# Optimization experiments

Measured on AMD Instinct MI355X. Metric: run time of the kernel, lower is better.

The kernel has to match this reference:

```python
import jax, jax.numpy as jnp
import numpy as np

AXIAL_WEIGHT = 1.0
N_NODES = 1_000_000
N_ELEM = 2_000_000


def setup_inputs() -> dict:
    key = jax.random.key(0)
    ks = jax.random.split(key, 12)
    N, E = N_NODES, N_ELEM
    pred_raw = jax.random.normal(ks[0], (N, 3), jnp.float32)
    u_c = jax.random.uniform(ks[1], (1,), jnp.float32) + 0.5
    theta_c = jax.random.uniform(ks[2], (1,), jnp.float32) + 0.5
    connectivity = jax.random.randint(ks[3], (E, 2), 0, N, jnp.int32)
    # lengths / section properties bounded away from zero (1/L^3 appears)
    elem_lengths = jax.random.uniform(ks[4], (E,), jnp.float32) + 0.5
    prop_E = jax.random.uniform(ks[5], (E,), jnp.float32) + 1.0
    prop_A = jax.random.uniform(ks[6], (E,), jnp.float32) + 0.5
    prop_I22 = jax.random.uniform(ks[7], (E,), jnp.float32) + 0.5
    ang = jax.random.uniform(ks[8], (E,), jnp.float32) * (2.0 * np.pi)
    # columns: [cos, 0, sin] -- forward reads cols 0 and 2
    elem_directions = jnp.stack([jnp.cos(ang), jnp.zeros_like(ang), jnp.sin(ang)], axis=1)
    F_ext = jax.random.normal(ks[9], (N, 3), jnp.float32)
    bc_disp = (jax.random.uniform(ks[10], (N, 1)) < 0.05).astype(jnp.float32)
    bc_rot = (jax.random.uniform(ks[11], (N, 1)) < 0.05).astype(jnp.float32)
    return {
        "pred_raw": pred_raw, "u_c": u_c, "theta_c": theta_c,
        "elem_lengths": elem_lengths, "prop_E": prop_E, "prop_A": prop_A,
        "prop_I22": prop_I22, "elem_directions": elem_directions,
        "F_ext": F_ext, "bc_disp": bc_disp, "bc_rot": bc_rot,
        "connectivity": connectivity,
    }


def reference(pred_raw, u_c, theta_c, elem_lengths, prop_E, prop_A, prop_I22,
              elem_directions, F_ext, bc_disp, bc_rot, connectivity):
    n_nodes = pred_raw.shape[0]
    # physical displacements: [ux*u_c, uz*u_c, th*theta_c]
    scale = jnp.concatenate([u_c, u_c, theta_c])  # [3]
    u_phys = pred_raw * scale[None, :]

    nA = connectivity[:, 0]
    nB = connectivity[:, 1]
    c = elem_directions[:, 0]
    s = elem_directions[:, 2]
    L = elem_lengths
    EA = prop_E * prop_A
    EI = prop_E * prop_I22

    uA = u_phys[nA]  # [E,3] gather
    uB = u_phys[nB]
    u_A = c * uA[:, 0] + s * uA[:, 1]
    w_A = -s * uA[:, 0] + c * uA[:, 1]
    th_A = -uA[:, 2]
    u_B = c * uB[:, 0] + s * uB[:, 1]
    w_B = -s * uB[:, 0] + c * uB[:, 1]
    th_B = -uB[:, 2]

    ea_l = EA / L * AXIAL_WEIGHT
    ei_l = EI / L
    ei_l2 = EI / L**2
    ei_l3 = EI / L**3

    # analytic K_loc @ d_local (K_loc is the standard 6x6 beam stiffness)
    dw = w_A - w_B
    f0 = ea_l * (u_A - u_B)
    f1 = 12.0 * ei_l3 * dw + 6.0 * ei_l2 * (th_A + th_B)
    f2 = 6.0 * ei_l2 * dw + 4.0 * ei_l * th_A + 2.0 * ei_l * th_B
    f3 = -f0
    f4 = -f1
    f5 = 6.0 * ei_l2 * dw + 2.0 * ei_l * th_A + 4.0 * ei_l * th_B

    fA = jnp.stack([c * f0 - s * f1, s * f0 + c * f1, -f2], axis=1)  # [E,3]
    fB = jnp.stack([c * f3 - s * f4, s * f3 + c * f4, -f5], axis=1)

    F_int = jax.ops.segment_sum(
        jnp.concatenate([fA, fB], axis=0),
        jnp.concatenate([nA, nB], axis=0),
        num_segments=n_nodes)  # [N,3] scatter-add

    R = F_int - F_ext
    free_mask = jnp.concatenate([1.0 - bc_disp, 1.0 - bc_disp, 1.0 - bc_rot], axis=1)
    R_free = R * free_mask
    F_free = F_ext * free_mask
    F_norm_sq = jnp.maximum(jnp.sum(F_free**2), 1e-30)
    loss = jnp.sum(R_free**2) / F_norm_sq  # single graph -> n_graphs = 1
    return loss
```

## Files before the change

kernel.cpp:

```cpp
#include <hip/hip_runtime.h>
#include <hip/hip_fp16.h>


#define SPANC  4096
#define NBC    256
#define CURP   4
#define FTH    1024
#define FBE    2048
#define CB     96
#define NCHUNK 4
#define BASEI  272
#define QSCALE 8192.0f
#define QINV   1.220703125e-4f

#define SMEM_BYTES 49408
#define FO_SLAB 0
#define FO_SBK  32768
#define FO_HIST 36864
#define FO_BOFF 37888
#define FO_AST  38912
#define FO_WSUM 39936
#define AO_TILE 0
#define AO_SN   49152
#define AO_SD   49280

__device__ __forceinline__ uint2 packrec(float fx, float fy, float fz, int local) {
    unsigned short hx = __half_as_ushort(__float2half(fx));
    unsigned short hy = __half_as_ushort(__float2half(fy));
    unsigned short hz = __half_as_ushort(__float2half(fz));
    return make_uint2(((unsigned)hy << 16) | hx, ((unsigned)local << 16) | hz);
}

__device__ __forceinline__ int block_incl_scan(int v, int* wsum, int lane, int wv) {
    #pragma unroll
    for (int off = 1; off < 64; off <<= 1) {
        int t = __shfl_up(v, off, 64);
        if (lane >= off) v += t;
    }
    if (lane == 63) wsum[wv] = v;
    __syncthreads();
    if (wv == 0) {
        int w = (lane < 16) ? wsum[lane] : 0;
        #pragma unroll
        for (int off = 1; off < 16; off <<= 1) {
            int t = __shfl_up(w, off, 64);
            if (lane >= off) w += t;
        }
        if (lane < 16) wsum[lane] = w;
    }
    __syncthreads();
    return v + ((wv > 0) ? wsum[wv - 1] : 0);
}

__global__ void __launch_bounds__(1024)
upcnt_kernel(const float* __restrict__ pred, const float* __restrict__ u_c,
             const float* __restrict__ theta_c, uint2* __restrict__ up,
             int N, int upG,
             const long long* __restrict__ conn, int* __restrict__ rows,
             int E, int CE) {
    __shared__ int h[NCHUNK][NBC];
    int tid = threadIdx.x;
    int bid = blockIdx.x;

    if (bid < upG) {
        int i = bid * 1024 + tid;
        if (i < N) {
            float uc = u_c[0], tc = theta_c[0];
            float x = __builtin_nontemporal_load(&pred[3 * i + 0]) * uc;
            float y = __builtin_nontemporal_load(&pred[3 * i + 1]) * uc;
            float z = __builtin_nontemporal_load(&pred[3 * i + 2]) * tc;
            unsigned hx = __half_as_ushort(__float2half(x));
            unsigned hy = __half_as_ushort(__float2half(y));
            unsigned hz = __half_as_ushort(__float2half(z));
            up[i] = make_uint2((hy << 16) | hx, hz);
        }
        return;
    }

    int blk = bid - upG;
    h[tid >> 8][tid & 255] = 0;
    __syncthreads();
    int stride = CB * 1024;
    int ce2 = 2 * CE, ce3 = 3 * CE;
    for (int e = blk * 1024 + tid; e < E; e += stride) {
        long long v = __builtin_nontemporal_load(conn + e);
        int na = (int)(unsigned)((unsigned long long)v & 0xFFFFFFFFull);
        int nb = (int)(unsigned)((unsigned long long)v >> 32);
        int c = (e >= ce2) ? ((e >= ce3) ? 3 : 2) : ((e >= CE) ? 1 : 0);
        atomicAdd(&h[c][na >> 12], 1);
        atomicAdd(&h[c][nb >> 12], 1);
    }
    __syncthreads();
    int c = tid >> 8, b = tid & 255;
    __builtin_nontemporal_store(h[c][b], &rows[(c * CB + blk) * NBC + b]);
}

__global__ void __launch_bounds__(1024)
scan4_kernel(const int* __restrict__ rows, int* __restrict__ cursors,
             int* __restrict__ bases, double* __restrict__ accSlots) {
    __shared__ int wsum[16];
    __shared__ int segend[NCHUNK];
    int tid = threadIdx.x, lane = tid & 63, wv = tid >> 6;
    int c = tid >> 8, b = tid & 255;
    int v = 0;
    #pragma unroll 4
    for (int r = 0; r < CB; ++r) v += rows[(c * CB + r) * NBC + b];
    int incl = block_incl_scan(v, wsum, lane, wv);
    if (b == 255) segend[c] = incl;
    __syncthreads();
    int segoff = (c > 0) ? segend[c - 1] : 0;
    int inclSeg = incl - segoff;
    int* base_c = bases + c * BASEI;
    base_c[b + 1] = inclSeg;
    if (b == 0) base_c[0] = 0;
    cursors[(c * NBC + b) * CURP] = inclSeg - v;
    if (tid < 512) accSlots[tid] = 0.0;
}

__device__ __forceinline__ void fill_body(
    char* smem,
    const long long* __restrict__ conn,
    const uint2* __restrict__ upk,
    const float* __restrict__ len,
    const float* __restrict__ pE,
    const float* __restrict__ pA,
    const float* __restrict__ pI,
    const float* __restrict__ dir,
    uint2* __restrict__ arena,
    int* __restrict__ cursor,
    int cs, int ce, int bid) {
    uint2*         slab   = (uint2*)(smem + FO_SLAB);
    unsigned char* sbk    = (unsigned char*)(smem + FO_SBK);
    int*           hist   = (int*)(smem + FO_HIST);
    int*           boff   = (int*)(smem + FO_BOFF);
    int*           astart = (int*)(smem + FO_AST);
    int*           wsum   = (int*)(smem + FO_WSUM);

    int tid = threadIdx.x, lane = tid & 63, wv = tid >> 6;
    if (tid < NBC) hist[tid] = 0;
    __syncthreads();

    int bs = cs + bid * FBE;
    int be = bs + FBE; if (be > ce) be = ce;

    unsigned sv[4];
    uint2    rc[4];

    #pragma unroll
    for (int j = 0; j < 2; ++j) {
        int e = bs + j * FTH + tid;
        unsigned sa = 0xFFFFFFFFu, sb = 0xFFFFFFFFu;
        if (e < be) {
            long long cv = __builtin_nontemporal_load(conn + e);
            int na = (int)(unsigned)((unsigned long long)cv & 0xFFFFFFFFull);
            int nb = (int)(unsigned)((unsigned long long)cv >> 32);

            uint2 ua = upk[na];
            uint2 ub = upk[nb];

            float c  = __builtin_nontemporal_load(&dir[3 * e + 0]);
            float s  = __builtin_nontemporal_load(&dir[3 * e + 2]);
            float L  = __builtin_nontemporal_load(&len[e]);
            float Ee = __builtin_nontemporal_load(&pE[e]);
            float EA = Ee * __builtin_nontemporal_load(&pA[e]);
            float EI = Ee * __builtin_nontemporal_load(&pI[e]);

            float a0 = __half2float(__ushort_as_half((unsigned short)(ua.x & 0xFFFFu)));
            float a1 = __half2float(__ushort_as_half((unsigned short)(ua.x >> 16)));
            float a2 = __half2float(__ushort_as_half((unsigned short)(ua.y & 0xFFFFu)));
            float b0 = __half2float(__ushort_as_half((unsigned short)(ub.x & 0xFFFFu)));
            float b1 = __half2float(__ushort_as_half((unsigned short)(ub.x >> 16)));
            float b2 = __half2float(__ushort_as_half((unsigned short)(ub.y & 0xFFFFu)));

            float u_A  =  c * a0 + s * a1;
            float w_A  = -s * a0 + c * a1;
            float th_A = -a2;
            float u_B  =  c * b0 + s * b1;
            float w_B  = -s * b0 + c * b1;
            float th_B = -b2;

            float invL  = 1.0f / L;
            float ea_l  = EA * invL;
            float ei_l  = EI * invL;
            float ei_l2 = ei_l  * invL;
            float ei_l3 = ei_l2 * invL;

            float dw = w_A - w_B;
            float f0 = ea_l * (u_A - u_B);
            float f1 = 12.0f * ei_l3 * dw + 6.0f * ei_l2 * (th_A + th_B);
            float f2 = 6.0f * ei_l2 * dw + 4.0f * ei_l * th_A + 2.0f * ei_l * th_B;
            float f5 = 6.0f * ei_l2 * dw + 2.0f * ei_l * th_A + 4.0f * ei_l * th_B;

            float fA0 = c * f0 - s * f1;
            float fA1 = s * f0 + c * f1;

            int bkA = na >> 12;
            int rA  = atomicAdd(&hist[bkA], 1);
            sa = ((unsigned)rA << 8) | (unsigned)bkA;
            rc[2 * j + 0] = packrec(fA0, fA1, -f2, na & 4095);

            int bkB = nb >> 12;
            int rB  = atomicAdd(&hist[bkB], 1);
            sb = ((unsigned)rB << 8) | (unsigned)bkB;
            rc[2 * j + 1] = packrec(-fA0, -fA1, -f5, nb & 4095);
        }
        sv[2 * j + 0] = sa;
        sv[2 * j + 1] = sb;
    }
    __syncthreads();

    int h = (tid < NBC) ? hist[tid] : 0;
    if (tid < NBC && h) astart[tid] = atomicAdd(&cursor[tid * CURP], h);
    int iT = block_incl_scan(h, wsum, lane, wv);
    if (tid < NBC) boff[tid] = iT - h;
    __syncthreads();

    #pragma unroll
    for (int r = 0; r < 4; ++r) {
        unsigned s2 = sv[r];
        if (s2 != 0xFFFFFFFFu) {
            int bk = (int)(s2 & 255u);
            int rk = (int)(s2 >> 8);
            int slot = boff[bk] + rk;
            slab[slot] = rc[r];
            sbk[slot]  = (unsigned char)bk;
        }
    }
    __syncthreads();

    int tot = boff[NBC - 1] + hist[NBC - 1];
    for (int i = tid; i < tot; i += FTH) {
        int bk = sbk[i];
        uint2 r2 = slab[i];
        unsigned long long v = ((unsigned long long)r2.y << 32) | (unsigned long long)r2.x;
        __builtin_nontemporal_store(v,
            (unsigned long long*)&arena[astart[bk] + (i - boff[bk])]);
    }
}

__device__ __forceinline__ void accum_body(
    char* smem,
    const unsigned long long* __restrict__ arena,
    const int* __restrict__ base,
    const float* __restrict__ Fext,
    const float* __restrict__ bcd,
    const float* __restrict__ bcr,
    double* __restrict__ accSlots,
    unsigned short* __restrict__ fint16,
    int N, int isFirst, int isLast, int b) {
    int*    tile = (int*)(smem + AO_TILE);
    double* sn   = (double*)(smem + AO_SN);
    double* sd   = (double*)(smem + AO_SD);

    int tid = threadIdx.x, lane = tid & 63, wv = tid >> 6;
    int nodeLo = b * SPANC;
    int gBase = nodeLo * 3;
    int gMax  = 3 * N;

    if (isFirst) {
        for (int i = tid; i < SPANC * 3; i += FTH) tile[i] = 0;
    } else {
        for (int i = tid; i < SPANC * 3; i += FTH) {
            int g = gBase + i;
            tile[i] = (g < gMax)
                ? __float2int_rn(__half2float(__ushort_as_half(
                      __builtin_nontemporal_load(&fint16[g]))) * QSCALE)
                : 0;
        }
    }
    __syncthreads();

    int s0 = base[b];
    int s1 = base[b + 1];
    for (int i = s0 + tid; i < s1; i += FTH) {
        unsigned long long rv = __builtin_nontemporal_load(arena + i);
        unsigned lo = (unsigned)(rv & 0xFFFFFFFFull);
        unsigned hi = (unsigned)(rv >> 32);
        float fx = __half2float(__ushort_as_half((unsigned short)(lo & 0xFFFFu)));
        float fy = __half2float(__ushort_as_half((unsigned short)(lo >> 16)));
        float fz = __half2float(__ushort_as_half((unsigned short)(hi & 0xFFFFu)));
        int local = (int)(hi >> 16);
        atomicAdd(&tile[local * 3 + 0], __float2int_rn(fx * QSCALE));
        atomicAdd(&tile[local * 3 + 1], __float2int_rn(fy * QSCALE));
        atomicAdd(&tile[local * 3 + 2], __float2int_rn(fz * QSCALE));
    }
    __syncthreads();

    if (!isLast) {
        for (int i = tid; i < SPANC * 3; i += FTH) {
            int g = gBase + i;
            if (g < gMax)
                __builtin_nontemporal_store(
                    __half_as_ushort(__float2half((float)tile[i] * QINV)),
                    &fint16[g]);
        }
        return;
    }

    int spanCnt = N - nodeLo;
    if (spanCnt > SPANC) spanCnt = SPANC;

    double num = 0.0, den = 0.0;
    for (int l = tid; l < spanCnt; l += FTH) {
        int n = nodeLo + l;
        float md = 1.0f - __builtin_nontemporal_load(&bcd[n]);
        float mr = 1.0f - __builtin_nontemporal_load(&bcr[n]);
        float e0 = __builtin_nontemporal_load(&Fext[3 * n + 0]);
        float e1 = __builtin_nontemporal_load(&Fext[3 * n + 1]);
        float e2 = __builtin_nontemporal_load(&Fext[3 * n + 2]);
        float t0 = (float)tile[l * 3 + 0] * QINV;
        float t1 = (float)tile[l * 3 + 1] * QINV;
        float t2 = (float)tile[l * 3 + 2] * QINV;
        float r0 = (t0 - e0) * md;
        float r1 = (t1 - e1) * md;
        float r2 = (t2 - e2) * mr;
        float g0 = e0 * md;
        float g1 = e1 * md;
        float g2 = e2 * mr;
        num += (double)r0 * r0 + (double)r1 * r1 + (double)r2 * r2;
        den += (double)g0 * g0 + (double)g1 * g1 + (double)g2 * g2;
    }
    #pragma unroll
    for (int off = 32; off > 0; off >>= 1) {
        num += __shfl_down(num, off, 64);
        den += __shfl_down(den, off, 64);
    }
    if (lane == 0) { sn[wv] = num; sd[wv] = den; }
    __syncthreads();
    if (tid == 0) {
        double tn = 0.0, td = 0.0;
        #pragma unroll
        for (int w = 0; w < 16; ++w) { tn += sn[w]; td += sd[w]; }
        double* slot = accSlots + (size_t)(b & 63) * 8;
        atomicAdd(&slot[0], tn);
        atomicAdd(&slot[1], td);
    }
}

__global__ void __launch_bounds__(1024)
fill_kernel(const long long* __restrict__ conn, const uint2* __restrict__ upk,
            const float* __restrict__ len, const float* __restrict__ pE,
            const float* __restrict__ pA, const float* __restrict__ pI,
            const float* __restrict__ dir, uint2* __restrict__ arena,
            int* __restrict__ cursor, int cs, int ce) {
    __shared__ __align__(16) char smem[SMEM_BYTES];
    fill_body(smem, conn, upk, len, pE, pA, pI, dir, arena, cursor, cs, ce,
              blockIdx.x);
}

__global__ void __launch_bounds__(1024)
accum_kernel(const unsigned long long* __restrict__ arena,
             const int* __restrict__ base, const float* __restrict__ Fext,
             const float* __restrict__ bcd, const float* __restrict__ bcr,
             double* __restrict__ accSlots, unsigned short* __restrict__ fint16,
             int N, int isFirst, int isLast) {
    __shared__ __align__(16) char smem[SMEM_BYTES];
    accum_body(smem, arena, base, Fext, bcd, bcr, accSlots, fint16, N,
               isFirst, isLast, blockIdx.x);
}

__global__ void __launch_bounds__(1024)
mid_kernel(const long long* __restrict__ conn, const uint2* __restrict__ upk,
           const float* __restrict__ len, const float* __restrict__ pE,
           const float* __restrict__ pA, const float* __restrict__ pI,
           const float* __restrict__ dir,
           uint2* __restrict__ arenaF, int* __restrict__ cursorF,
           int csF, int ceF, int NTF,
           const unsigned long long* __restrict__ arenaA,
           const int* __restrict__ baseA,
           const float* __restrict__ Fext, const float* __restrict__ bcd,
           const float* __restrict__ bcr, double* __restrict__ accSlots,
           unsigned short* __restrict__ fint16, int N, int isFirstA) {
    __shared__ __align__(16) char smem[SMEM_BYTES];
    if ((int)blockIdx.x < NTF)
        fill_body(smem, conn, upk, len, pE, pA, pI, dir, arenaF, cursorF,
                  csF, ceF, blockIdx.x);
    else
        accum_body(smem, arenaA, baseA, Fext, bcd, bcr, accSlots, fint16, N,
                   isFirstA, 0, blockIdx.x - NTF);
}

__global__ void final_kernel(const double* __restrict__ accSlots,
                             float* __restrict__ out) {
    int t = threadIdx.x;
    double n = accSlots[t * 8 + 0];
    double d = accSlots[t * 8 + 1];
    #pragma unroll
    for (int off = 32; off > 0; off >>= 1) {
        n += __shfl_down(n, off, 64);
        d += __shfl_down(d, off, 64);
    }
    if (t == 0) {
        if (d < 1e-30) d = 1e-30;
        out[0] = (float)(n / d);
    }
}

static inline size_t align256(size_t x) { return (x + 255) & ~(size_t)255; }

extern "C" void kernel_launch(void* const* d_in, const int* in_sizes, int n_in,
                              void* d_out, int out_size, void* d_ws, size_t ws_size,
                              hipStream_t stream) {
    const float* pred    = (const float*)d_in[0];
    const float* u_c     = (const float*)d_in[1];
    const float* theta_c = (const float*)d_in[2];
    const float* len     = (const float*)d_in[3];
    const float* pE      = (const float*)d_in[4];
    const float* pA      = (const float*)d_in[5];
    const float* pI      = (const float*)d_in[6];
    const float* dir     = (const float*)d_in[7];
    const float* Fext    = (const float*)d_in[8];
    const float* bcd     = (const float*)d_in[9];
    const float* bcr     = (const float*)d_in[10];
    const long long* conn = (const long long*)d_in[11];

    int N = in_sizes[0] / 3;
    int E = in_sizes[3];
    int NBc = (N + SPANC - 1) / SPANC;
    int CE  = (E + NCHUNK - 1) / NCHUNK;
    int nCh = (E + CE - 1) / CE;
    int upG = (N + 1023) / 1024;

    size_t oCur  = 4096;
    size_t oBase = oCur + (size_t)NCHUNK * NBC * CURP * 4;
    size_t oU    = align256(oBase + (size_t)NCHUNK * BASEI * 4);
    size_t oFint = align256(oU + (size_t)N * 8);
    size_t oA0   = align256(oFint + (size_t)3 * N * 2);
    size_t arenaB = (size_t)2 * CE * 8;
    size_t rowsB  = (size_t)NCHUNK * CB * NBC * 4;
    size_t a0B    = (arenaB > rowsB) ? arenaB : rowsB;
    size_t oA1    = align256(oA0 + a0B);
    int fused = (oA1 + arenaB) <= ws_size;

    double*             accSlots = (double*)d_ws;
    int*                cursors  = (int*)((char*)d_ws + oCur);
    int*                bases    = (int*)((char*)d_ws + oBase);
    uint2*              upk      = (uint2*)((char*)d_ws + oU);
    unsigned short*     fint16   = (unsigned short*)((char*)d_ws + oFint);
    uint2*              arena0   = (uint2*)((char*)d_ws + oA0);
    uint2*              arena1   = (uint2*)((char*)d_ws + oA1);
    int*                rows     = (int*)arena0;

    upcnt_kernel<<<upG + CB, 1024, 0, stream>>>(
        pred, u_c, theta_c, upk, N, upG, conn, rows, E, CE);
    scan4_kernel<<<1, 1024, 0, stream>>>(rows, cursors, bases, accSlots);

    if (fused) {
        {
            int cs = 0, ce = (CE < E) ? CE : E;
            int NT = (ce - cs + FBE - 1) / FBE;
            fill_kernel<<<NT, FTH, 0, stream>>>(
                conn, upk, len, pE, pA, pI, dir,
                arena0, cursors + 0, 0, ce);
        }
        for (int c = 1; c < nCh; ++c) {
            int cs = c * CE;
            int ce = cs + CE; if (ce > E) ce = E;
            int NT = (ce - cs + FBE - 1) / FBE;
            uint2* aF = (c & 1) ? arena1 : arena0;
            const unsigned long long* aA = (const unsigned long long*)
                (((c - 1) & 1) ? arena1 : arena0);
            mid_kernel<<<NT + NBc, FTH, 0, stream>>>(
                conn, upk, len, pE, pA, pI, dir,
                aF, cursors + (size_t)c * NBC * CURP, cs, ce, NT,
                aA, bases + (size_t)(c - 1) * BASEI,
                Fext, bcd, bcr, accSlots, fint16, N, (c - 1) == 0);
        }
        {
            int last = nCh - 1;
            const unsigned long long* aA = (const unsigned long long*)
                ((last & 1) ? arena1 : arena0);
            accum_kernel<<<NBc, FTH, 0, stream>>>(
                aA, bases + (size_t)last * BASEI,
                Fext, bcd, bcr, accSlots, fint16, N, last == 0, 1);
        }
    } else {
        for (int c = 0; c < nCh; ++c) {
            int cs = c * CE;
            int ce = cs + CE; if (ce > E) ce = E;
            int NT = (ce - cs + FBE - 1) / FBE;
            fill_kernel<<<NT, FTH, 0, stream>>>(
                conn, upk, len, pE, pA, pI, dir,
                arena0, cursors + (size_t)c * NBC * CURP, cs, ce);
            accum_kernel<<<NBc, FTH, 0, stream>>>(
                (const unsigned long long*)arena0, bases + (size_t)c * BASEI,
                Fext, bcd, bcr, accSlots, fint16, N, c == 0, c == nCh - 1);
        }
    }

    final_kernel<<<1, 64, 0, stream>>>(accSlots, (float*)d_out);
}
```

Measured before the change: 260.3 us.

## Drop fused fill/accumulate overlap; pick fewer, larger chunks to fit workspace

Removes mid_kernel, which overlapped filling chunk c with accumulating chunk c-1 through double-buffered arenas. It goes back to a single arena with sequential fill and accum launches per chunk, and picks the smallest chunk count (2, 3 or 4) whose arena fits the workspace. Fewer chunks means fewer launches and fewer fint16 round trips, but each accum pass now waits on its fill with no overlap. Per-kernel shared memory is now sized per kernel rather than one union buffer, which may change occupancy. Note that the scan and histogram still index four chunks (tid>>8), while the chunk boundaries now come from K; this is consistent only if upcnt uses the passed CE.

```diff
diff --git a/kernel.cpp b/kernel.cpp
--- a/kernel.cpp
+++ b/kernel.cpp
@@ -8,21 +8,10 @@
 #define FTH    1024
 #define FBE    2048
 #define CB     96
-#define NCHUNK 4
+#define NCHMAX 4
 #define BASEI  272
 #define QSCALE 8192.0f
 #define QINV   1.220703125e-4f
-
-#define SMEM_BYTES 49408
-#define FO_SLAB 0
-#define FO_SBK  32768
-#define FO_HIST 36864
-#define FO_BOFF 37888
-#define FO_AST  38912
-#define FO_WSUM 39936
-#define AO_TILE 0
-#define AO_SN   49152
-#define AO_SD   49280
 
 __device__ __forceinline__ uint2 packrec(float fx, float fy, float fz, int local) {
     unsigned short hx = __half_as_ushort(__float2half(fx));
@@ -58,7 +47,7 @@
              int N, int upG,
              const long long* __restrict__ conn, int* __restrict__ rows,
              int E, int CE) {
-    __shared__ int h[NCHUNK][NBC];
+    __shared__ int h[NCHMAX][NBC];
     int tid = threadIdx.x;
     int bid = blockIdx.x;
 
@@ -99,7 +88,7 @@
 scan4_kernel(const int* __restrict__ rows, int* __restrict__ cursors,
              int* __restrict__ bases, double* __restrict__ accSlots) {
     __shared__ int wsum[16];
-    __shared__ int segend[NCHUNK];
+    __shared__ int segend[NCHMAX];
     int tid = threadIdx.x, lane = tid & 63, wv = tid >> 6;
     int c = tid >> 8, b = tid & 255;
     int v = 0;
@@ -117,30 +106,30 @@
     if (tid < 512) accSlots[tid] = 0.0;
 }
 
-__device__ __forceinline__ void fill_body(
-    char* smem,
-    const long long* __restrict__ conn,
-    const uint2* __restrict__ upk,
-    const float* __restrict__ len,
-    const float* __restrict__ pE,
-    const float* __restrict__ pA,
-    const float* __restrict__ pI,
-    const float* __restrict__ dir,
-    uint2* __restrict__ arena,
-    int* __restrict__ cursor,
-    int cs, int ce, int bid) {
-    uint2*         slab   = (uint2*)(smem + FO_SLAB);
-    unsigned char* sbk    = (unsigned char*)(smem + FO_SBK);
-    int*           hist   = (int*)(smem + FO_HIST);
-    int*           boff   = (int*)(smem + FO_BOFF);
-    int*           astart = (int*)(smem + FO_AST);
-    int*           wsum   = (int*)(smem + FO_WSUM);
+__global__ void __launch_bounds__(1024)
+fill_kernel(const long long* __restrict__ conn,
+            const uint2* __restrict__ upk,
+            const float* __restrict__ len,
+            const float* __restrict__ pE,
+            const float* __restrict__ pA,
+            const float* __restrict__ pI,
+            const float* __restrict__ dir,
+            uint2* __restrict__ arena,
+            int* __restrict__ cursor,
+            int cs, int ce) {
+    __shared__ uint2         slab[2 * FBE];
+    __shared__ unsigned char sbk [2 * FBE];
+    __shared__ int hist [NBC];
+    __shared__ int boff [NBC];
+    __shared__ int astart[NBC];
+    __shared__ int wsum [16];
 
     int tid = threadIdx.x, lane = tid & 63, wv = tid >> 6;
+
     if (tid < NBC) hist[tid] = 0;
     __syncthreads();
 
-    int bs = cs + bid * FBE;
+    int bs = cs + blockIdx.x * FBE;
     int be = bs + FBE; if (be > ce) be = ce;
 
     unsigned sv[4];
@@ -238,21 +227,20 @@
     }
 }
 
-__device__ __forceinline__ void accum_body(
-    char* smem,
-    const unsigned long long* __restrict__ arena,
-    const int* __restrict__ base,
-    const float* __restrict__ Fext,
-    const float* __restrict__ bcd,
-    const float* __restrict__ bcr,
-    double* __restrict__ accSlots,
-    unsigned short* __restrict__ fint16,
-    int N, int isFirst, int isLast, int b) {
-    int*    tile = (int*)(smem + AO_TILE);
-    double* sn   = (double*)(smem + AO_SN);
-    double* sd   = (double*)(smem + AO_SD);
+__global__ void __launch_bounds__(1024)
+accum_kernel(const unsigned long long* __restrict__ arena,
+             const int* __restrict__ base,
+             const float* __restrict__ Fext,
+             const float* __restrict__ bcd,
+             const float* __restrict__ bcr,
+             double* __restrict__ accSlots,
+             unsigned short* __restrict__ fint16,
+             int N, int isFirst, int isLast) {
+    __shared__ int tile[SPANC * 3];
+    __shared__ double sn[16], sd[16];
 
     int tid = threadIdx.x, lane = tid & 63, wv = tid >> 6;
+    int b = blockIdx.x;
     int nodeLo = b * SPANC;
     int gBase = nodeLo * 3;
     int gMax  = 3 * N;
@@ -337,49 +325,6 @@
     }
 }
 
-__global__ void __launch_bounds__(1024)
-fill_kernel(const long long* __restrict__ conn, const uint2* __restrict__ upk,
-            const float* __restrict__ len, const float* __restrict__ pE,
-            const float* __restrict__ pA, const float* __restrict__ pI,
-            const float* __restrict__ dir, uint2* __restrict__ arena,
-            int* __restrict__ cursor, int cs, int ce) {
-    __shared__ __align__(16) char smem[SMEM_BYTES];
-    fill_body(smem, conn, upk, len, pE, pA, pI, dir, arena, cursor, cs, ce,
-              blockIdx.x);
-}
-
-__global__ void __launch_bounds__(1024)
-accum_kernel(const unsigned long long* __restrict__ arena,
-             const int* __restrict__ base, const float* __restrict__ Fext,
-             const float* __restrict__ bcd, const float* __restrict__ bcr,
-             double* __restrict__ accSlots, unsigned short* __restrict__ fint16,
-             int N, int isFirst, int isLast) {
-    __shared__ __align__(16) char smem[SMEM_BYTES];
-    accum_body(smem, arena, base, Fext, bcd, bcr, accSlots, fint16, N,
-               isFirst, isLast, blockIdx.x);
-}
-
-__global__ void __launch_bounds__(1024)
-mid_kernel(const long long* __restrict__ conn, const uint2* __restrict__ upk,
-           const float* __restrict__ len, const float* __restrict__ pE,
-           const float* __restrict__ pA, const float* __restrict__ pI,
-           const float* __restrict__ dir,
-           uint2* __restrict__ arenaF, int* __restrict__ cursorF,
-           int csF, int ceF, int NTF,
-           const unsigned long long* __restrict__ arenaA,
-           const int* __restrict__ baseA,
-           const float* __restrict__ Fext, const float* __restrict__ bcd,
-           const float* __restrict__ bcr, double* __restrict__ accSlots,
-           unsigned short* __restrict__ fint16, int N, int isFirstA) {
-    __shared__ __align__(16) char smem[SMEM_BYTES];
-    if ((int)blockIdx.x < NTF)
-        fill_body(smem, conn, upk, len, pE, pA, pI, dir, arenaF, cursorF,
-                  csF, ceF, blockIdx.x);
-    else
-        accum_body(smem, arenaA, baseA, Fext, bcd, bcr, accSlots, fint16, N,
-                   isFirstA, 0, blockIdx.x - NTF);
-}
-
 __global__ void final_kernel(const double* __restrict__ accSlots,
                              float* __restrict__ out) {
     int t = threadIdx.x;
@@ -417,75 +362,48 @@
     int N = in_sizes[0] / 3;
     int E = in_sizes[3];
     int NBc = (N + SPANC - 1) / SPANC;
-    int CE  = (E + NCHUNK - 1) / NCHUNK;
+    int upG = (N + 1023) / 1024;
+
+    size_t oCur  = 4096;
+    size_t oBase = oCur + (size_t)NCHMAX * NBC * CURP * 4;
+    size_t oU    = align256(oBase + (size_t)NCHMAX * BASEI * 4);
+    size_t oFint = align256(oU + (size_t)N * 8);
+    size_t oA    = align256(oFint + (size_t)3 * N * 2);
+    size_t rowsB = (size_t)NCHMAX * CB * NBC * 4;
+
+    const int cfgK[3] = {2, 3, 4};
+    int K = 4;
+    for (int t = 0; t < 3; ++t) {
+        size_t chunkE = (size_t)(E + cfgK[t] - 1) / cfgK[t];
+        size_t arenaB = 2 * chunkE * 8;
+        if (arenaB < rowsB) arenaB = rowsB;
+        if (oA + arenaB <= ws_size || t == 2) { K = cfgK[t]; if (oA + arenaB <= ws_size) break; }
+    }
+    int CE  = (E + K - 1) / K;
     int nCh = (E + CE - 1) / CE;
-    int upG = (N + 1023) / 1024;
-
-    size_t oCur  = 4096;
-    size_t oBase = oCur + (size_t)NCHUNK * NBC * CURP * 4;
-    size_t oU    = align256(oBase + (size_t)NCHUNK * BASEI * 4);
-    size_t oFint = align256(oU + (size_t)N * 8);
-    size_t oA0   = align256(oFint + (size_t)3 * N * 2);
-    size_t arenaB = (size_t)2 * CE * 8;
-    size_t rowsB  = (size_t)NCHUNK * CB * NBC * 4;
-    size_t a0B    = (arenaB > rowsB) ? arenaB : rowsB;
-    size_t oA1    = align256(oA0 + a0B);
-    int fused = (oA1 + arenaB) <= ws_size;
 
     double*             accSlots = (double*)d_ws;
     int*                cursors  = (int*)((char*)d_ws + oCur);
     int*                bases    = (int*)((char*)d_ws + oBase);
     uint2*              upk      = (uint2*)((char*)d_ws + oU);
     unsigned short*     fint16   = (unsigned short*)((char*)d_ws + oFint);
-    uint2*              arena0   = (uint2*)((char*)d_ws + oA0);
-    uint2*              arena1   = (uint2*)((char*)d_ws + oA1);
-    int*                rows     = (int*)arena0;
+    uint2*              arena    = (uint2*)((char*)d_ws + oA);
+    int*                rows     = (int*)arena;
 
     upcnt_kernel<<<upG + CB, 1024, 0, stream>>>(
         pred, u_c, theta_c, upk, N, upG, conn, rows, E, CE);
     scan4_kernel<<<1, 1024, 0, stream>>>(rows, cursors, bases, accSlots);
 
-    if (fused) {
-        {
-            int cs = 0, ce = (CE < E) ? CE : E;
-            int NT = (ce - cs + FBE - 1) / FBE;
-            fill_kernel<<<NT, FTH, 0, stream>>>(
-                conn, upk, len, pE, pA, pI, dir,
-                arena0, cursors + 0, 0, ce);
-        }
-        for (int c = 1; c < nCh; ++c) {
-            int cs = c * CE;
-            int ce = cs + CE; if (ce > E) ce = E;
-            int NT = (ce - cs + FBE - 1) / FBE;
-            uint2* aF = (c & 1) ? arena1 : arena0;
-            const unsigned long long* aA = (const unsigned long long*)
-                (((c - 1) & 1) ? arena1 : arena0);
-            mid_kernel<<<NT + NBc, FTH, 0, stream>>>(
-                conn, upk, len, pE, pA, pI, dir,
-                aF, cursors + (size_t)c * NBC * CURP, cs, ce, NT,
-                aA, bases + (size_t)(c - 1) * BASEI,
-                Fext, bcd, bcr, accSlots, fint16, N, (c - 1) == 0);
-        }
-        {
-            int last = nCh - 1;
-            const unsigned long long* aA = (const unsigned long long*)
-                ((last & 1) ? arena1 : arena0);
-            accum_kernel<<<NBc, FTH, 0, stream>>>(
-                aA, bases + (size_t)last * BASEI,
-                Fext, bcd, bcr, accSlots, fint16, N, last == 0, 1);
-        }
-    } else {
-        for (int c = 0; c < nCh; ++c) {
-            int cs = c * CE;
-            int ce = cs + CE; if (ce > E) ce = E;
-            int NT = (ce - cs + FBE - 1) / FBE;
-            fill_kernel<<<NT, FTH, 0, stream>>>(
-                conn, upk, len, pE, pA, pI, dir,
-                arena0, cursors + (size_t)c * NBC * CURP, cs, ce);
-            accum_kernel<<<NBc, FTH, 0, stream>>>(
-                (const unsigned long long*)arena0, bases + (size_t)c * BASEI,
-                Fext, bcd, bcr, accSlots, fint16, N, c == 0, c == nCh - 1);
-        }
+    for (int c = 0; c < nCh; ++c) {
+        int cs = c * CE;
+        int ce = cs + CE; if (ce > E) ce = E;
+        int NT = (ce - cs + FBE - 1) / FBE;
+        fill_kernel<<<NT, FTH, 0, stream>>>(
+            conn, upk, len, pE, pA, pI, dir,
+            arena, cursors + (size_t)c * NBC * CURP, cs, ce);
+        accum_kernel<<<NBc, FTH, 0, stream>>>(
+            (const unsigned long long*)arena, bases + (size_t)c * BASEI,
+            Fext, bcd, bcr, accSlots, fint16, N, c == 0, c == nCh - 1);
     }
 
     final_kernel<<<1, 64, 0, stream>>>(accSlots, (float*)d_out);
```

Measured after the change: 236.8 us. 9.0% less time.
